# Optimization experiments

Hardware: AMD Instinct MI355X
Metric: run time of the kernel (lower is better)

Reference implementation:

```python
import jax, jax.numpy as jnp
import numpy as np

TOP_K = 2

def _mlp(x, w_gate_up, b_gate_up, w_down):
    # x: [T,H]; w_gate_up: [2I,H]; b_gate_up: [2I]; w_down: [H,I]
    gu = x @ w_gate_up.T + b_gate_up
    i = w_gate_up.shape[0] // 2
    h = jax.nn.silu(gu[..., :i]) * gu[..., i:]  # SiluAndMul
    return h @ w_down.T

def setup_inputs() -> dict:
    key = jax.random.key(0)
    ks = jax.random.split(key, 8)
    T, H, I, E = 8192, 1024, 512, 16
    s = 0.02  # weight init scale
    return {
        "hidden_states": jax.random.normal(ks[0], (T, H), jnp.float32),
        "gate_w": jax.random.normal(ks[1], (E, H), jnp.float32) * s,
        "w_gate_up": jax.random.normal(ks[2], (E, 2 * I, H), jnp.float32) * s,
        "b_gate_up": jax.random.normal(ks[3], (E, 2 * I), jnp.float32) * s,
        "w_down": jax.random.normal(ks[4], (E, H, I), jnp.float32) * s,
        "ws_gate_up": jax.random.normal(ks[5], (2 * I, H), jnp.float32) * s,
        "bs_gate_up": jax.random.normal(ks[6], (2 * I,), jnp.float32) * s,
        "ws_down": jax.random.normal(ks[7], (H, I), jnp.float32) * s,
    }

def reference(hidden_states, gate_w, w_gate_up, b_gate_up, w_down,
              ws_gate_up, bs_gate_up, ws_down):
    x = hidden_states  # [T,H]
    E = gate_w.shape[0]

    # shared expert
    shared_out = _mlp(x, ws_gate_up, bs_gate_up, ws_down)  # [T,H]

    # router: softmax in float32, then top-k and renormalize (norm_topk_prob)
    router_logits = x @ gate_w.T  # [T,E]
    probs = jax.nn.softmax(router_logits.astype(jnp.float32), axis=-1)
    rw, sel = jax.lax.top_k(probs, TOP_K)  # [T,K]
    rw = rw / jnp.sum(rw, axis=-1, keepdims=True)

    # per-token per-expert weight [T,E] (0 for unselected experts)
    ew = jnp.sum(jax.nn.one_hot(sel, E, dtype=rw.dtype) * rw[..., None], axis=1)

    # dense all-experts MLP (faithful to the naive masked loop, vectorized)
    gu = jnp.einsum('th,eih->eti', x, w_gate_up) + b_gate_up[:, None, :]  # [E,T,2I]
    I = gu.shape[-1] // 2
    act = jax.nn.silu(gu[..., :I]) * gu[..., I:]  # [E,T,I]
    # scaling by routing weight commutes with the linear down_proj
    wact = act * ew.T[:, :, None].astype(act.dtype)  # [E,T,I]
    final = jnp.einsum('eti,ehi->th', wact, w_down)  # [T,H]

    return final + shared_out
```

## Files before the change

kernel.cpp:

```cpp
#include <hip/hip_runtime.h>
#include <hip/hip_bf16.h>
#include <cstdint>
#include <cstddef>

typedef _Float16 f16;
typedef _Float16 f16x4 __attribute__((ext_vector_type(4)));
typedef _Float16 f16x8 __attribute__((ext_vector_type(8)));
typedef float f32x4 __attribute__((ext_vector_type(4)));

#define GPTR(p) ((const __attribute__((address_space(1))) void*)(p))
#define LPTR(p) ((__attribute__((address_space(3))) void*)(p))

#define T_TOK 8192
#define H_DIM 1024
#define I_DIM 512
#define N_EXP 16
#define N_ALL 17
#define TOPK 2
#define NSLOT (T_TOK * TOPK)
#define NSLOT_ALL (NSLOT + T_TOK)

#define MAX_TILES 208
#define XCD_TILES (MAX_TILES / 8)

#define PREP_BLOCKS 42530
__global__ void prep_kernel(const float* __restrict__ x, const float* __restrict__ gw,
                            const float* __restrict__ wgu, const float* __restrict__ wsgu,
                            const float* __restrict__ wd, const float* __restrict__ wsd,
                            const float* __restrict__ bgu, const float* __restrict__ bsgu,
                            f16* __restrict__ x_h, f16* __restrict__ x_l,
                            f16* __restrict__ gw_h, f16* __restrict__ gw_l,
                            f16* __restrict__ wguA, f16* __restrict__ wdA,
                            float* __restrict__ biasA, int* __restrict__ counts,
                            float* __restrict__ out0) {
    const int bid = blockIdx.x, tid = threadIdx.x;
    if (bid < 8192) {
        int i = bid * 256 + tid;
        float4 v = ((const float4*)x)[i];
        float vv[4] = { v.x, v.y, v.z, v.w };
        f16x4 h, l;
#pragma unroll
        for (int r = 0; r < 4; r++) { h[r] = (f16)vv[r]; l[r] = (f16)(vv[r] - (float)h[r]); }
        *(f16x4*)(x_h + (size_t)i * 4) = h;
        *(f16x4*)(x_l + (size_t)i * 4) = l;
    } else if (bid < 8208) {
        int i = (bid - 8192) * 256 + tid;
        float4 v = ((const float4*)gw)[i];
        float vv[4] = { v.x, v.y, v.z, v.w };
        f16x4 h, l;
#pragma unroll
        for (int r = 0; r < 4; r++) { h[r] = (f16)vv[r]; l[r] = (f16)(vv[r] - (float)h[r]); }
        *(f16x4*)(gw_h + (size_t)i * 4) = h;
        *(f16x4*)(gw_l + (size_t)i * 4) = l;
    } else if (bid < 24592) {
        int i = (bid - 8208) * 256 + tid;
        float4 v = ((const float4*)wgu)[i];
        f16x4 o = { (f16)v.x, (f16)v.y, (f16)v.z, (f16)v.w };
        *(f16x4*)(wguA + (size_t)i * 4) = o;
    } else if (bid < 25616) {
        int i = (bid - 24592) * 256 + tid;
        float4 v = ((const float4*)wsgu)[i];
        f16x4 o = { (f16)v.x, (f16)v.y, (f16)v.z, (f16)v.w };
        *(f16x4*)(wguA + (size_t)16 * 1024 * 1024 + (size_t)i * 4) = o;
    } else if (bid < 33808) {
        int i = (bid - 25616) * 256 + tid;
        float4 v = ((const float4*)wd)[i];
        f16x4 o = { (f16)v.x, (f16)v.y, (f16)v.z, (f16)v.w };
        *(f16x4*)(wdA + (size_t)i * 4) = o;
    } else if (bid < 34320) {
        int i = (bid - 33808) * 256 + tid;
        float4 v = ((const float4*)wsd)[i];
        f16x4 o = { (f16)v.x, (f16)v.y, (f16)v.z, (f16)v.w };
        *(f16x4*)(wdA + (size_t)16 * 1024 * 512 + (size_t)i * 4) = o;
    } else if (bid < 34336) {
        int i = (bid - 34320) * 256 + tid;
        ((float4*)biasA)[i] = ((const float4*)bgu)[i];
    } else if (bid == 34336) {
        ((float4*)(biasA + 16384))[tid] = ((const float4*)bsgu)[tid];
    } else if (bid == 34337) {
        if (tid < 16) counts[tid] = 0;
    } else {
        size_t i = (size_t)(bid - 34338) * 256 + tid;
        ((float4*)out0)[i] = (float4){0.f, 0.f, 0.f, 0.f};
    }
}

__global__ __launch_bounds__(256) void logits_kernel(
    const f16* __restrict__ Xh, const f16* __restrict__ Xl,
    const f16* __restrict__ Gh, const f16* __restrict__ Gl,
    float* __restrict__ L) {
    const int wave = threadIdx.x >> 6, lane = threadIdx.x & 63;
    const int m0 = blockIdx.x * 64 + wave * 16;
    const int qm = lane & 15, quad = lane >> 4;
    const size_t arow = (size_t)(m0 + qm) * H_DIM + quad * 8;
    const size_t brow = (size_t)qm * H_DIM + quad * 8;
    f32x4 acc = (f32x4){0.f, 0.f, 0.f, 0.f};
    const f16* ap;
    const f16* bp;
    ap = Xh + arow; bp = Gh + brow;
#pragma unroll 8
    for (int k0 = 0; k0 < H_DIM; k0 += 32) {
        acc = __builtin_amdgcn_mfma_f32_16x16x32_f16(*(const f16x8*)ap, *(const f16x8*)bp, acc, 0, 0, 0);
        ap += 32; bp += 32;
    }
    ap = Xh + arow; bp = Gl + brow;
#pragma unroll 8
    for (int k0 = 0; k0 < H_DIM; k0 += 32) {
        acc = __builtin_amdgcn_mfma_f32_16x16x32_f16(*(const f16x8*)ap, *(const f16x8*)bp, acc, 0, 0, 0);
        ap += 32; bp += 32;
    }
    ap = Xl + arow; bp = Gh + brow;
#pragma unroll 8
    for (int k0 = 0; k0 < H_DIM; k0 += 32) {
        acc = __builtin_amdgcn_mfma_f32_16x16x32_f16(*(const f16x8*)ap, *(const f16x8*)bp, acc, 0, 0, 0);
        ap += 32; bp += 32;
    }
#pragma unroll
    for (int r = 0; r < 4; r++)
        L[(size_t)(m0 + quad * 4 + r) * N_EXP + qm] = acc[r];
}

__global__ void topk_kernel(const float* __restrict__ L, int* __restrict__ sel,
                            float* __restrict__ rw, int* __restrict__ counts) {
    __shared__ int lc[N_EXP];
    const int tid = threadIdx.x;
    if (tid < N_EXP) lc[tid] = 0;
    __syncthreads();
    const int t = blockIdx.x * 256 + tid;
    float lg[16];
    const float4* lp = (const float4*)(L + (size_t)t * N_EXP);
#pragma unroll
    for (int q = 0; q < 4; q++) {
        float4 v = lp[q];
        lg[q * 4 + 0] = v.x; lg[q * 4 + 1] = v.y; lg[q * 4 + 2] = v.z; lg[q * 4 + 3] = v.w;
    }
    float best = -1e30f, sec = -1e30f; int bi = 0, si = 0;
#pragma unroll
    for (int j = 0; j < 16; j++) {
        float lj = lg[j];
        if (lj > best) { sec = best; si = bi; best = lj; bi = j; }
        else if (lj > sec) { sec = lj; si = j; }
    }
    float w1 = 1.f / (1.f + __expf(sec - best));
    sel[t * 2] = bi; sel[t * 2 + 1] = si;
    rw[t * 2] = w1;  rw[t * 2 + 1] = 1.f - w1;
    atomicAdd(&lc[bi], 1);
    atomicAdd(&lc[si], 1);
    __syncthreads();
    if (tid < N_EXP) atomicAdd(&counts[tid], lc[tid]);
}

__global__ void prefix_kernel(const int* __restrict__ counts, int* __restrict__ offsets,
                              int* __restrict__ cursors, int* __restrict__ tiles) {
    if (threadIdx.x == 0) {
        int s = 0;
        for (int e = 0; e < N_EXP; e++) { offsets[e] = s; cursors[e] = s; s += counts[e]; }
        offsets[N_EXP] = s;
        offsets[N_EXP + 1] = s + T_TOK;
        int nt = 0;
        for (int m0 = 0; m0 < T_TOK; m0 += 128) tiles[nt++] = (16 << 20) | m0;
        for (int e = 0; e < N_EXP; e++) {
            int M = counts[e];
            for (int m0 = 0; m0 < M; m0 += 128) tiles[nt++] = (e << 20) | m0;
        }
        for (; nt < MAX_TILES; nt++) tiles[nt] = -1;
    }
}

__global__ void scatter_kernel(const int* __restrict__ sel, const float* __restrict__ rw,
                               int* __restrict__ cursors, int* __restrict__ btok,
                               float* __restrict__ bw) {
    int t = blockIdx.x * blockDim.x + threadIdx.x;
    if (t >= T_TOK) return;
#pragma unroll
    for (int k = 0; k < TOPK; k++) {
        int e = sel[t * 2 + k];
        int p = atomicAdd(&cursors[e], 1);
        btok[p] = t;
        bw[p] = rw[t * 2 + k];
    }
    btok[NSLOT + t] = t;
    bw[NSLOT + t] = 1.f;
}

__device__ __forceinline__ void xcd_tile_map(int g, int& ti, int& n0i) {
    const int x = g & 7;
    const int q = g >> 3;
    ti  = x * XCD_TILES + (q >> 3);
    n0i = q & 7;
}

#define WAITV4_BAR() do { \
    asm volatile("s_waitcnt vmcnt(4)" ::: "memory"); \
    __builtin_amdgcn_s_barrier(); } while (0)
#define WAITV0_BAR() do { \
    asm volatile("s_waitcnt vmcnt(0)" ::: "memory"); \
    __builtin_amdgcn_s_barrier(); } while (0)

__global__ __launch_bounds__(256, 4) void gemm_gateup_act(
    const f16* __restrict__ X,
    const f16* __restrict__ W,
    const float* __restrict__ bias,
    const float* __restrict__ bw,
    f16* __restrict__ ACT,
    const int* __restrict__ offsets,
    const int* __restrict__ btok,
    const int* __restrict__ tiles) {
    constexpr int K = H_DIM;
    constexpr int NT = K / 32;
    int ti, n0i;
    xcd_tile_map(blockIdx.x, ti, n0i);
    const int td = tiles[ti];
    if (td < 0) return;
    const int e  = td >> 20;
    const int m0 = td & 0xFFFFF;
    const int n0 = n0i * 64;
    const int base = offsets[e];
    const int M = offsets[e + 1] - base;

    const f16* Wb   = W + (size_t)e * 1024 * K;
    const float* bb = bias + (size_t)e * 1024;

    __shared__ f16 As[2][128 * 32];
    __shared__ f16 Bg[2][64 * 32];
    __shared__ f16 Bu[2][64 * 32];

    const int tid  = threadIdx.x;
    const int wave = tid >> 6;
    const int lane = tid & 63;
    const int srow = lane >> 2;
    const int csw  = ((lane & 3) ^ ((srow >> 1) & 3)) * 8;

    int ar0 = m0 + wave * 32 + srow;
    int ar1 = ar0 + 16;
    int r0 = min(ar0, M - 1), r1 = min(ar1, M - 1);
    const f16* ap0 = X + (size_t)btok[base + r0] * K + csw;
    const f16* ap1 = X + (size_t)btok[base + r1] * K + csw;
    const int brow = n0 + wave * 16 + srow;
    const f16* bg0 = Wb + (size_t)brow * K + csw;
    const f16* bu0 = bg0 + (size_t)512 * K;
    f16* la0 = &As[0][(wave * 32) * 32];
    f16* la1 = la0 + 16 * 32;
    f16* lg0 = &Bg[0][(wave * 16) * 32];
    f16* lu0 = &Bu[0][(wave * 16) * 32];
    constexpr int AST = 128 * 32;
    constexpr int BST = 64 * 32;

    const int wm = (wave >> 1) * 64;
    const int wn = (wave & 1) * 32;
    const int qm = lane & 15;
    const int quad = lane >> 4;
    const int qsw = (quad ^ ((qm >> 1) & 3)) * 8;

    f32x4 accg[4][2], accu[4][2];
#pragma unroll
    for (int i = 0; i < 4; i++)
#pragma unroll
        for (int j = 0; j < 2; j++) {
            accg[i][j] = (f32x4){0.f, 0.f, 0.f, 0.f};
            accu[i][j] = (f32x4){0.f, 0.f, 0.f, 0.f};
        }

#define GU_STAGE(b) do { \
    __builtin_amdgcn_global_load_lds(GPTR(ap0), LPTR(la0 + (b) * AST), 16, 0, 0); \
    __builtin_amdgcn_global_load_lds(GPTR(ap1), LPTR(la1 + (b) * AST), 16, 0, 0); \
    __builtin_amdgcn_global_load_lds(GPTR(bg0), LPTR(lg0 + (b) * BST), 16, 0, 0); \
    __builtin_amdgcn_global_load_lds(GPTR(bu0), LPTR(lu0 + (b) * BST), 16, 0, 0); \
    ap0 += 32; ap1 += 32; bg0 += 32; bu0 += 32; } while (0)

#define GU_COMPUTE(b) do { \
    f16x8 af[4], gf[2], uf[2]; \
    _Pragma("unroll") \
    for (int i = 0; i < 4; i++) af[i] = *(const f16x8*)&As[b][(wm + i * 16 + qm) * 32 + qsw]; \
    _Pragma("unroll") \
    for (int j = 0; j < 2; j++) { \
        gf[j] = *(const f16x8*)&Bg[b][(wn + j * 16 + qm) * 32 + qsw]; \
        uf[j] = *(const f16x8*)&Bu[b][(wn + j * 16 + qm) * 32 + qsw]; \
    } \
    _Pragma("unroll") \
    for (int i = 0; i < 4; i++) \
        _Pragma("unroll") \
        for (int j = 0; j < 2; j++) { \
            accg[i][j] = __builtin_amdgcn_mfma_f32_16x16x32_f16(af[i], gf[j], accg[i][j], 0, 0, 0); \
            accu[i][j] = __builtin_amdgcn_mfma_f32_16x16x32_f16(af[i], uf[j], accu[i][j], 0, 0, 0); \
        } } while (0)

    GU_STAGE(0);
    for (int t = 0; t < NT; t += 2) {
        __builtin_amdgcn_s_barrier();
        GU_STAGE(1);
        WAITV4_BAR();
        GU_COMPUTE(0);
        __builtin_amdgcn_s_barrier();
        if (t + 2 < NT) {
            GU_STAGE(0);
            WAITV4_BAR();
        } else {
            WAITV0_BAR();
        }
        GU_COMPUTE(1);
    }

#pragma unroll
    for (int i = 0; i < 4; i++) {
#pragma unroll
        for (int j = 0; j < 2; j++) {
            const int colg = n0 + wn + j * 16 + qm;
            const float bvg = bb[colg];
            const float bvu = bb[colg + 512];
#pragma unroll
            for (int r = 0; r < 4; r++) {
                const int lr = wm + i * 16 + quad * 4 + r;
                const int m = m0 + lr;
                if (m < M) {
                    float g = accg[i][j][r] + bvg;
                    float u = accu[i][j][r] + bvu;
                    float sl = g / (1.f + __expf(-g));
                    ACT[(size_t)(base + m) * 512 + colg] = (f16)(sl * u * bw[base + m]);
                }
            }
        }
    }
}

__global__ __launch_bounds__(256, 4) void gemm_down(
    const f16* __restrict__ ACT,
    const f16* __restrict__ W,
    float* __restrict__ OUT,
    const int* __restrict__ offsets,
    const int* __restrict__ btok,
    const int* __restrict__ tiles) {
    constexpr int K = I_DIM;
    constexpr int NT = K / 32;
    int ti, n0i;
    xcd_tile_map(blockIdx.x, ti, n0i);
    const int td = tiles[ti];
    if (td < 0) return;
    const int e  = td >> 20;
    const int m0 = td & 0xFFFFF;
    const int n0 = n0i * 128;
    const int base = offsets[e];
    const int M = offsets[e + 1] - base;

    const f16* Wb = W + (size_t)e * 1024 * K;

    __shared__ f16 As[2][128 * 32];
    __shared__ f16 Bs[2][128 * 32];

    const int tid  = threadIdx.x;
    const int wave = tid >> 6;
    const int lane = tid & 63;
    const int srow = lane >> 2;
    const int csw  = ((lane & 3) ^ ((srow >> 1) & 3)) * 8;

    int ar0 = m0 + wave * 32 + srow;
    int ar1 = ar0 + 16;
    int r0 = min(ar0, M - 1), r1 = min(ar1, M - 1);
    const f16* ap0 = ACT + (size_t)(base + r0) * K + csw;
    const f16* ap1 = ACT + (size_t)(base + r1) * K + csw;
    const f16* bp0 = Wb + (size_t)(n0 + wave * 32 + srow) * K + csw;
    const f16* bp1 = bp0 + (size_t)16 * K;
    f16* la0 = &As[0][(wave * 32) * 32];  f16* la1 = la0 + 16 * 32;
    f16* lb0 = &Bs[0][(wave * 32) * 32];  f16* lb1 = lb0 + 16 * 32;
    constexpr int DST = 128 * 32;

    const int wm = (wave >> 1) * 64;
    const int wn = (wave & 1) * 64;
    const int qm = lane & 15;
    const int quad = lane >> 4;
    const int qsw = (quad ^ ((qm >> 1) & 3)) * 8;

    f32x4 acc[4][4];
#pragma unroll
    for (int i = 0; i < 4; i++)
#pragma unroll
        for (int j = 0; j < 4; j++) acc[i][j] = (f32x4){0.f, 0.f, 0.f, 0.f};

#define DN_STAGE(b) do { \
    __builtin_amdgcn_global_load_lds(GPTR(ap0), LPTR(la0 + (b) * DST), 16, 0, 0); \
    __builtin_amdgcn_global_load_lds(GPTR(ap1), LPTR(la1 + (b) * DST), 16, 0, 0); \
    __builtin_amdgcn_global_load_lds(GPTR(bp0), LPTR(lb0 + (b) * DST), 16, 0, 0); \
    __builtin_amdgcn_global_load_lds(GPTR(bp1), LPTR(lb1 + (b) * DST), 16, 0, 0); \
    ap0 += 32; ap1 += 32; bp0 += 32; bp1 += 32; } while (0)

#define DN_COMPUTE(b) do { \
    f16x8 af[4], bfr[4]; \
    _Pragma("unroll") \
    for (int i = 0; i < 4; i++) af[i]  = *(const f16x8*)&As[b][(wm + i * 16 + qm) * 32 + qsw]; \
    _Pragma("unroll") \
    for (int j = 0; j < 4; j++) bfr[j] = *(const f16x8*)&Bs[b][(wn + j * 16 + qm) * 32 + qsw]; \
    _Pragma("unroll") \
    for (int i = 0; i < 4; i++) \
        _Pragma("unroll") \
        for (int j = 0; j < 4; j++) \
            acc[i][j] = __builtin_amdgcn_mfma_f32_16x16x32_f16(af[i], bfr[j], acc[i][j], 0, 0, 0); \
    } while (0)

    DN_STAGE(0);
    for (int t = 0; t < NT; t += 2) {
        __builtin_amdgcn_s_barrier();
        DN_STAGE(1);
        WAITV4_BAR();
        DN_COMPUTE(0);
        __builtin_amdgcn_s_barrier();
        if (t + 2 < NT) {
            DN_STAGE(0);
            WAITV4_BAR();
        } else {
            WAITV0_BAR();
        }
        DN_COMPUTE(1);
    }

#pragma unroll
    for (int i = 0; i < 4; i++) {
#pragma unroll
        for (int r = 0; r < 4; r++) {
            const int lr = wm + i * 16 + quad * 4 + r;
            const int m = m0 + lr;
            if (m < M) {
                const int tok = btok[base + m];
                float* orow = OUT + (size_t)tok * 1024 + n0 + wn + qm;
#pragma unroll
                for (int j = 0; j < 4; j++)
                    atomicAdd(orow + j * 16, acc[i][j][r]);
            }
        }
    }
}

extern "C" void kernel_launch(void* const* d_in, const int* in_sizes, int n_in,
                              void* d_out, int out_size, void* d_ws, size_t ws_size,
                              hipStream_t stream) {
    const float* x    = (const float*)d_in[0];
    const float* gw   = (const float*)d_in[1];
    const float* wgu  = (const float*)d_in[2];
    const float* bgu  = (const float*)d_in[3];
    const float* wd   = (const float*)d_in[4];
    const float* wsgu = (const float*)d_in[5];
    const float* bsgu = (const float*)d_in[6];
    const float* wsd  = (const float*)d_in[7];
    float* out = (float*)d_out;

    char* ws = (char*)d_ws;
    size_t off = 0;
    auto take = [&](size_t b) { char* p = ws + off; off = (off + b + 255) & ~(size_t)255; return p; };
    f16* x_h    = (f16*)take((size_t)T_TOK * H_DIM * 2);
    f16* x_l    = (f16*)take((size_t)T_TOK * H_DIM * 2);
    f16* gw_h   = (f16*)take((size_t)N_EXP * H_DIM * 2);
    f16* gw_l   = (f16*)take((size_t)N_EXP * H_DIM * 2);
    f16* wguA   = (f16*)take((size_t)N_ALL * 1024 * H_DIM * 2);
    f16* wdA    = (f16*)take((size_t)N_ALL * 1024 * I_DIM * 2);
    float* biasA = (float*)take((size_t)N_ALL * 1024 * 4);
    f16* act    = (f16*)take((size_t)NSLOT_ALL * I_DIM * 2);
    float* logits = (float*)take((size_t)T_TOK * N_EXP * 4);
    int*   sel    = (int*)take((size_t)NSLOT * 4);
    float* rw     = (float*)take((size_t)NSLOT * 4);
    int*   btok   = (int*)take((size_t)NSLOT_ALL * 4);
    float* bw     = (float*)take((size_t)NSLOT_ALL * 4);
    int*   counts = (int*)take(64);
    int*   offs   = (int*)take(128);
    int*   curs   = (int*)take(64);
    int*   tiles  = (int*)take(MAX_TILES * 4);

    prep_kernel<<<PREP_BLOCKS, 256, 0, stream>>>(x, gw, wgu, wsgu, wd, wsd, bgu, bsgu,
                                                 x_h, x_l, gw_h, gw_l, wguA, wdA, biasA,
                                                 counts, out);

    logits_kernel<<<T_TOK / 64, 256, 0, stream>>>(x_h, x_l, gw_h, gw_l, logits);
    topk_kernel<<<T_TOK / 256, 256, 0, stream>>>(logits, sel, rw, counts);
    prefix_kernel<<<1, 64, 0, stream>>>(counts, offs, curs, tiles);
    scatter_kernel<<<T_TOK / 256, 256, 0, stream>>>(sel, rw, curs, btok, bw);

    gemm_gateup_act<<<dim3(MAX_TILES * 8, 1, 1), 256, 0, stream>>>(x_h, wguA, biasA, bw, act, offs, btok, tiles);

    gemm_down<<<dim3(MAX_TILES * 8, 1, 1), 256, 0, stream>>>(act, wdA, out, offs, btok, tiles);
}
```

Baseline: 427.0 us.

## Replace atomic scatter-add in down GEMM with fp16 staging and gather combine

The down-projection GEMM now writes per-slot results as fp16 into a slot-ordered buffer instead of atomically adding fp32 values into the output by token. A new combine kernel gathers each token's shared-expert row and its two routed-expert rows using recorded slot positions, then writes the summed output directly. This also removes the output zeroing from the prep kernel. It avoids about 25M fp32 atomics but adds a 50MB fp16 intermediate write and read, plus an extra launch, and rounds partial results to fp16 before summation.

```diff
diff --git a/kernel.cpp b/kernel.cpp
--- a/kernel.cpp
+++ b/kernel.cpp
@@ -23,7 +23,7 @@
 #define MAX_TILES 208
 #define XCD_TILES (MAX_TILES / 8)
 
-#define PREP_BLOCKS 42530
+#define PREP_BLOCKS 34338
 __global__ void prep_kernel(const float* __restrict__ x, const float* __restrict__ gw,
                             const float* __restrict__ wgu, const float* __restrict__ wsgu,
                             const float* __restrict__ wd, const float* __restrict__ wsd,
@@ -31,8 +31,7 @@
                             f16* __restrict__ x_h, f16* __restrict__ x_l,
                             f16* __restrict__ gw_h, f16* __restrict__ gw_l,
                             f16* __restrict__ wguA, f16* __restrict__ wdA,
-                            float* __restrict__ biasA, int* __restrict__ counts,
-                            float* __restrict__ out0) {
+                            float* __restrict__ biasA, int* __restrict__ counts) {
     const int bid = blockIdx.x, tid = threadIdx.x;
     if (bid < 8192) {
         int i = bid * 256 + tid;
@@ -77,11 +76,8 @@
         ((float4*)biasA)[i] = ((const float4*)bgu)[i];
     } else if (bid == 34336) {
         ((float4*)(biasA + 16384))[tid] = ((const float4*)bsgu)[tid];
-    } else if (bid == 34337) {
+    } else {
         if (tid < 16) counts[tid] = 0;
-    } else {
-        size_t i = (size_t)(bid - 34338) * 256 + tid;
-        ((float4*)out0)[i] = (float4){0.f, 0.f, 0.f, 0.f};
     }
 }
 
@@ -169,7 +165,7 @@
 
 __global__ void scatter_kernel(const int* __restrict__ sel, const float* __restrict__ rw,
                                int* __restrict__ cursors, int* __restrict__ btok,
-                               float* __restrict__ bw) {
+                               float* __restrict__ bw, int* __restrict__ pos) {
     int t = blockIdx.x * blockDim.x + threadIdx.x;
     if (t >= T_TOK) return;
 #pragma unroll
@@ -178,6 +174,7 @@
         int p = atomicAdd(&cursors[e], 1);
         btok[p] = t;
         bw[p] = rw[t * 2 + k];
+        pos[t * 2 + k] = p;
     }
     btok[NSLOT + t] = t;
     bw[NSLOT + t] = 1.f;
@@ -326,9 +323,8 @@
 __global__ __launch_bounds__(256, 4) void gemm_down(
     const f16* __restrict__ ACT,
     const f16* __restrict__ W,
-    float* __restrict__ OUT,
+    f16* __restrict__ DOWN,
     const int* __restrict__ offsets,
-    const int* __restrict__ btok,
     const int* __restrict__ tiles) {
     constexpr int K = I_DIM;
     constexpr int NT = K / 32;
@@ -415,18 +411,38 @@
 #pragma unroll
     for (int i = 0; i < 4; i++) {
 #pragma unroll
-        for (int r = 0; r < 4; r++) {
-            const int lr = wm + i * 16 + quad * 4 + r;
-            const int m = m0 + lr;
-            if (m < M) {
-                const int tok = btok[base + m];
-                float* orow = OUT + (size_t)tok * 1024 + n0 + wn + qm;
-#pragma unroll
-                for (int j = 0; j < 4; j++)
-                    atomicAdd(orow + j * 16, acc[i][j][r]);
+        for (int j = 0; j < 4; j++) {
+            const int col = n0 + wn + j * 16 + qm;
+#pragma unroll
+            for (int r = 0; r < 4; r++) {
+                const int lr = wm + i * 16 + quad * 4 + r;
+                const int m = m0 + lr;
+                if (m < M) DOWN[(size_t)(base + m) * 1024 + col] = (f16)acc[i][j][r];
             }
         }
     }
+}
+
+__global__ void combine_kernel(const f16* __restrict__ DOWN, const int* __restrict__ pos,
+                               float* __restrict__ OUT) {
+    int idx = blockIdx.x * blockDim.x + threadIdx.x;
+    int t = idx >> 7;
+    int c = (idx & 127) * 8;
+    int p1 = pos[t * 2], p2 = pos[t * 2 + 1];
+    f16x8 a = *(const f16x8*)(DOWN + (size_t)(NSLOT + t) * 1024 + c);
+    f16x8 b = *(const f16x8*)(DOWN + (size_t)p1 * 1024 + c);
+    f16x8 d = *(const f16x8*)(DOWN + (size_t)p2 * 1024 + c);
+    float4 o0, o1;
+    o0.x = (float)a[0] + (float)b[0] + (float)d[0];
+    o0.y = (float)a[1] + (float)b[1] + (float)d[1];
+    o0.z = (float)a[2] + (float)b[2] + (float)d[2];
+    o0.w = (float)a[3] + (float)b[3] + (float)d[3];
+    o1.x = (float)a[4] + (float)b[4] + (float)d[4];
+    o1.y = (float)a[5] + (float)b[5] + (float)d[5];
+    o1.z = (float)a[6] + (float)b[6] + (float)d[6];
+    o1.w = (float)a[7] + (float)b[7] + (float)d[7];
+    *(float4*)(OUT + (size_t)t * 1024 + c) = o0;
+    *(float4*)(OUT + (size_t)t * 1024 + c + 4) = o1;
 }
 
 extern "C" void kernel_launch(void* const* d_in, const int* in_sizes, int n_in,
@@ -453,26 +469,29 @@
     f16* wdA    = (f16*)take((size_t)N_ALL * 1024 * I_DIM * 2);
     float* biasA = (float*)take((size_t)N_ALL * 1024 * 4);
     f16* act    = (f16*)take((size_t)NSLOT_ALL * I_DIM * 2);
+    f16* down   = (f16*)take((size_t)NSLOT_ALL * 1024 * 2);
     float* logits = (float*)take((size_t)T_TOK * N_EXP * 4);
     int*   sel    = (int*)take((size_t)NSLOT * 4);
     float* rw     = (float*)take((size_t)NSLOT * 4);
     int*   btok   = (int*)take((size_t)NSLOT_ALL * 4);
     float* bw     = (float*)take((size_t)NSLOT_ALL * 4);
+    int*   pos    = (int*)take((size_t)NSLOT * 4);
     int*   counts = (int*)take(64);
     int*   offs   = (int*)take(128);
     int*   curs   = (int*)take(64);
     int*   tiles  = (int*)take(MAX_TILES * 4);
 
     prep_kernel<<<PREP_BLOCKS, 256, 0, stream>>>(x, gw, wgu, wsgu, wd, wsd, bgu, bsgu,
-                                                 x_h, x_l, gw_h, gw_l, wguA, wdA, biasA,
-                                                 counts, out);
+                                                 x_h, x_l, gw_h, gw_l, wguA, wdA, biasA, counts);
 
     logits_kernel<<<T_TOK / 64, 256, 0, stream>>>(x_h, x_l, gw_h, gw_l, logits);
     topk_kernel<<<T_TOK / 256, 256, 0, stream>>>(logits, sel, rw, counts);
     prefix_kernel<<<1, 64, 0, stream>>>(counts, offs, curs, tiles);
-    scatter_kernel<<<T_TOK / 256, 256, 0, stream>>>(sel, rw, curs, btok, bw);
+    scatter_kernel<<<T_TOK / 256, 256, 0, stream>>>(sel, rw, curs, btok, bw, pos);
 
     gemm_gateup_act<<<dim3(MAX_TILES * 8, 1, 1), 256, 0, stream>>>(x_h, wguA, biasA, bw, act, offs, btok, tiles);
 
-    gemm_down<<<dim3(MAX_TILES * 8, 1, 1), 256, 0, stream>>>(act, wdA, out, offs, btok, tiles);
-}
+    gemm_down<<<dim3(MAX_TILES * 8, 1, 1), 256, 0, stream>>>(act, wdA, down, offs, tiles);
+
+    combine_kernel<<<T_TOK * 1024 / 8 / 256, 256, 0, stream>>>(down, pos, out);
+}
```

After: 380.7 us. 10.9% less time.
